# Optimization experiments

Measured on AMD Instinct MI355X. Metric: run time of the kernel, lower is better.

The kernel has to match this reference:

```python
import jax, jax.numpy as jnp
import numpy as np

E = 1024      # embed_dim
H = 8         # att_heads
ALPHA = 1.3   # CELU alpha
EPS = 1e-5    # GroupNorm eps (torch default)


def _celu(x):
    return jnp.where(x > 0, x, ALPHA * jnp.expm1(x / ALPHA))


def _proj(x2d, W, b, gamma, beta):
    # Linear -> CELU(1.3) -> GroupNorm(H groups) over flattened tokens [N, E]
    y = x2d @ W.T + b
    y = _celu(y)
    N, C = y.shape
    yg = y.reshape(N, H, C // H)
    mu = yg.mean(-1, keepdims=True)
    var = yg.var(-1, keepdims=True)
    yn = ((yg - mu) * jax.lax.rsqrt(var + EPS)).reshape(N, C)
    return yn * gamma + beta


def setup_inputs() -> dict:
    key = jax.random.key(0)
    ks = jax.random.split(key, 16)
    B, M = 32, 1024
    inp = {
        'query':  jax.random.normal(ks[0], (B, M, E), jnp.float32),
        'key':    jax.random.normal(ks[1], (B, M, E), jnp.float32),
        'mask':   jnp.ones((B, M), jnp.int32),
        'value1': jax.random.normal(ks[2], (B, E), jnp.float32),
        'value2': jax.random.normal(ks[3], (B, M, E), jnp.float32),
    }
    def lin(k):
        return jax.random.normal(k, (E, E), jnp.float32) * 0.02
    inp.update({
        'Wq': lin(ks[4]),  'bq': jnp.zeros((E,), jnp.float32),
        'gq': jnp.ones((E,), jnp.float32), 'betaq': jnp.zeros((E,), jnp.float32),
        'Wk': lin(ks[5]),  'bk': jnp.zeros((E,), jnp.float32),
        'gk': jnp.ones((E,), jnp.float32), 'betak': jnp.zeros((E,), jnp.float32),
        'Wv': lin(ks[6]),  'bv': jnp.zeros((E,), jnp.float32),
        'gv': jnp.ones((E,), jnp.float32), 'betav': jnp.zeros((E,), jnp.float32),
        'Wm': lin(ks[7]),  'bm': jnp.zeros((E,), jnp.float32),
    })
    return inp


def reference(query, key, mask, value1, value2,
              Wq, bq, gq, betaq,
              Wk, bk, gk, betak,
              Wv, bv, gv, betav,
              Wm, bm):
    B, M, C = query.shape
    D = C // H
    scaling = D ** -0.5
    # value1 is intentionally unused (matches the original module)
    q = _proj(query.reshape(-1, C),  Wq, bq, gq, betaq).reshape(B, M, H, D).transpose(0, 2, 1, 3)
    k = _proj(key.reshape(-1, C),    Wk, bk, gk, betak).reshape(B, M, H, D).transpose(0, 2, 1, 3)
    v = _proj(value2.reshape(-1, C), Wv, bv, gv, betav).reshape(B, M, H, D).transpose(0, 2, 1, 3)
    scores = jnp.einsum('bhqd,bhkd->bhqk', q, k) * scaling
    scores = jnp.where(mask[:, None, None, :] == 0, jnp.float32(-1e9), scores)
    att = jax.nn.softmax(scores, axis=-1)
    out = jnp.einsum('bhqk,bhkd->bhqd', att, v)
    out = out.transpose(0, 2, 1, 3).reshape(B, M, C)
    return out @ Wm.T + bm
```

## Files before the change

### kernel.cpp

```cpp
#include <hip/hip_runtime.h>
#include <math.h>

#define E_DIM 1024
#define HH 8
#define DH 128
#define BB 32
#define MM 1024
#define NTOK 32768
#define CHUNK 16384
#define CELU_A 1.3f
#define GN_EPS 1e-5f
#define SCALE_F 0.08838834764831845f

typedef unsigned short ushort_t;
typedef __attribute__((ext_vector_type(8))) short short8;
typedef __attribute__((ext_vector_type(4))) float f32x4;

#define MFMA16(a,b,c) __builtin_amdgcn_mfma_f32_16x16x32_bf16((a),(b),(c),0,0,0)

union U8 { short8 v; ushort_t u[8]; };

__device__ __forceinline__ ushort_t f2bf(float f) {
    unsigned u = __float_as_uint(f);
    u += 0x7fffu + ((u >> 16) & 1u);
    return (ushort_t)(u >> 16);
}
__device__ __forceinline__ float bf2f(ushort_t h) {
    return __uint_as_float(((unsigned)h) << 16);
}

__device__ __forceinline__ void gload16(const void* g, void* l) {
    __builtin_amdgcn_global_load_lds(
        (const __attribute__((address_space(1))) unsigned*)g,
        (__attribute__((address_space(3))) unsigned*)l, 16, 0, 0);
}

__global__ __launch_bounds__(256)
void split_kernel(const float* __restrict__ in, ushort_t* __restrict__ hi,
                  ushort_t* __restrict__ lo, int n8)
{
    int i = blockIdx.x * 256 + threadIdx.x;
    if (i >= n8) return;
    const float4* p = (const float4*)in;
    float4 a = p[2 * i], b = p[2 * i + 1];
    float f[8] = {a.x, a.y, a.z, a.w, b.x, b.y, b.z, b.w};
    U8 h, l;
#pragma unroll
    for (int j = 0; j < 8; ++j) {
        ushort_t hh = f2bf(f[j]);
        h.u[j] = hh;
        l.u[j] = f2bf(f[j] - bf2f(hh));
    }
    *(short8*)&hi[(size_t)i * 8] = h.v;
    *(short8*)&lo[(size_t)i * 8] = l.v;
}

__global__ __launch_bounds__(32)
void pack_mask(const int* __restrict__ mask, unsigned* __restrict__ mbits)
{
    int b = blockIdx.x, t = threadIdx.x;
    const int* mp = mask + (size_t)b * MM + t * 32;
    unsigned v = 0;
    for (int j = 0; j < 32; ++j) v |= (mp[j] != 0 ? 1u : 0u) << j;
    mbits[b * 32 + t] = v;
}

struct alignas(16) TilesT {
    ushort_t ahi[128 * 32]; ushort_t alo[128 * 32];
    ushort_t bhi[128 * 32]; ushort_t blo[128 * 32];
};
struct alignas(16) EpiT {
    float ybuf[64 * 132]; float mu[64]; float rs[64];
};
union SmemU { TilesT t; EpiT e; };

template<int MODE>
__global__ __launch_bounds__(256, 3)
void proj_kernel(const ushort_t* __restrict__ Ahi, const ushort_t* __restrict__ Alo,
                 const ushort_t* __restrict__ Bhi, const ushort_t* __restrict__ Blo,
                 const float* __restrict__ bias, const float* __restrict__ gamma,
                 const float* __restrict__ beta, int row_off,
                 ushort_t* __restrict__ out0, ushort_t* __restrict__ out1,
                 float* __restrict__ outf)
{
    __shared__ SmemU sm;

    const int tid  = threadIdx.x;
    const int w    = tid >> 6, lane = tid & 63;
    const int quad = lane >> 4, l16 = lane & 15;
    const int wr   = (w >> 1) * 64, wc = (w & 1) * 64;
    const int lrow0 = blockIdx.x * 128;
    const int row0  = row_off + lrow0;
    const int col0  = blockIdx.y * 128;

    f32x4 Cf[4][4];
#pragma unroll
    for (int i = 0; i < 4; ++i)
#pragma unroll
        for (int j = 0; j < 4; ++j) Cf[i][j] = (f32x4){0.f, 0.f, 0.f, 0.f};

    const int s0 = tid, s1 = tid + 256;
    const int ra0 = tid >> 2, ra1 = ra0 + 64;
    const int ga  = (tid & 3) * 8;

    unsigned aoff0 = 0, aoff1 = 0;
    size_t a2b0 = 0, a2b1 = 0;
    if constexpr (MODE == 2) {
        int n0 = row0 + ra0, n1 = row0 + ra1;
        a2b0 = ((size_t)(n0 >> 10) * (HH * MM) + (n0 & 1023)) * 256;
        a2b1 = ((size_t)(n1 >> 10) * (HH * MM) + (n1 & 1023)) * 256;
    } else {
        aoff0 = (unsigned)((lrow0 + ra0) * E_DIM + ga);
        aoff1 = (unsigned)((lrow0 + ra1) * E_DIM + ga);
    }
    const unsigned boff0 = (unsigned)((col0 + ra0) * E_DIM + ga);
    const unsigned boff1 = (unsigned)((col0 + ra1) * E_DIM + ga);

    for (int k0 = 0; k0 < E_DIM; k0 += 32) {
        if constexpr (MODE == 2) {
            int e0 = k0 + ga;
            size_t ao = (size_t)(e0 >> 7) * (MM * 256) + (e0 & 127);
            gload16(Ahi + a2b0 + ao,       &sm.t.ahi[s0 * 8]);
            gload16(Ahi + a2b0 + ao + 128, &sm.t.alo[s0 * 8]);
            gload16(Ahi + a2b1 + ao,       &sm.t.ahi[s1 * 8]);
            gload16(Ahi + a2b1 + ao + 128, &sm.t.alo[s1 * 8]);
        } else {
            gload16(Ahi + aoff0 + k0, &sm.t.ahi[s0 * 8]);
            gload16(Alo + aoff0 + k0, &sm.t.alo[s0 * 8]);
            gload16(Ahi + aoff1 + k0, &sm.t.ahi[s1 * 8]);
            gload16(Alo + aoff1 + k0, &sm.t.alo[s1 * 8]);
        }
        gload16(Bhi + boff0 + k0, &sm.t.bhi[s0 * 8]);
        gload16(Blo + boff0 + k0, &sm.t.blo[s0 * 8]);
        gload16(Bhi + boff1 + k0, &sm.t.bhi[s1 * 8]);
        gload16(Blo + boff1 + k0, &sm.t.blo[s1 * 8]);
        __syncthreads();
        short8 a_hi[4], a_lo[4], b_hi[4], b_lo[4];
#pragma unroll
        for (int mt = 0; mt < 4; ++mt) {
            int r = wr + mt * 16 + l16;
            a_hi[mt] = *(const short8*)&sm.t.ahi[r * 32 + quad * 8];
            a_lo[mt] = *(const short8*)&sm.t.alo[r * 32 + quad * 8];
        }
#pragma unroll
        for (int nt = 0; nt < 4; ++nt) {
            int r = wc + nt * 16 + l16;
            b_hi[nt] = *(const short8*)&sm.t.bhi[r * 32 + quad * 8];
            b_lo[nt] = *(const short8*)&sm.t.blo[r * 32 + quad * 8];
        }
#pragma unroll
        for (int mt = 0; mt < 4; ++mt)
#pragma unroll
            for (int nt = 0; nt < 4; ++nt) {
                f32x4 c = Cf[mt][nt];
                c = MFMA16(a_hi[mt], b_hi[nt], c);
                c = MFMA16(a_hi[mt], b_lo[nt], c);
                c = MFMA16(a_lo[mt], b_hi[nt], c);
                Cf[mt][nt] = c;
            }
        __syncthreads();
    }

    if constexpr (MODE == 2) {
#pragma unroll
        for (int mt = 0; mt < 4; ++mt)
#pragma unroll
            for (int nt = 0; nt < 4; ++nt) {
                int c = col0 + wc + nt * 16 + l16;
                float bv = bias[c];
#pragma unroll
                for (int reg = 0; reg < 4; ++reg) {
                    int r = row0 + wr + mt * 16 + quad * 4 + reg;
                    outf[(size_t)r * E_DIM + c] = Cf[mt][nt][reg] + bv;
                }
            }
    } else {
        for (int h2 = 0; h2 < 2; ++h2) {
            __syncthreads();
            if ((w >> 1) == h2) {
#pragma unroll
                for (int mt = 0; mt < 4; ++mt)
#pragma unroll
                    for (int nt = 0; nt < 4; ++nt) {
                        int c = wc + nt * 16 + l16;
                        float bv = bias[col0 + c];
#pragma unroll
                        for (int reg = 0; reg < 4; ++reg) {
                            int r = mt * 16 + quad * 4 + reg;
                            float x = Cf[mt][nt][reg] + bv;
                            x = x > 0.f ? x : CELU_A * (__expf(x * (1.0f / CELU_A)) - 1.0f);
                            sm.e.ybuf[r * 132 + c] = x;
                        }
                    }
            }
            __syncthreads();
            {
                int r = tid >> 2, sg = (tid & 3) * 32;
                float s = 0.f, ss = 0.f;
                for (int i = 0; i < 32; i += 4) {
                    float4 v = *(float4*)&sm.e.ybuf[r * 132 + sg + i];
                    s  += v.x + v.y + v.z + v.w;
                    ss += v.x * v.x + v.y * v.y + v.z * v.z + v.w * v.w;
                }
                s  += __shfl_xor(s, 1);  ss += __shfl_xor(ss, 1);
                s  += __shfl_xor(s, 2);  ss += __shfl_xor(ss, 2);
                if ((tid & 3) == 0) {
                    float mu  = s * (1.f / 128.f);
                    float var = ss * (1.f / 128.f) - mu * mu;
                    sm.e.mu[r] = mu;
                    sm.e.rs[r] = rsqrtf(var + GN_EPS);
                }
            }
            __syncthreads();
            if constexpr (MODE == 0) {
                int r = tid >> 2, sg = (tid & 3) * 32;
                int n = row0 + h2 * 64 + r, b = n >> 10, m = n & 1023, h = blockIdx.y;
                float mu = sm.e.mu[r], rs = sm.e.rs[r];
                ushort_t* orow = out0 + ((size_t)((b * HH + h) * MM + m)) * 256;
                for (int i0 = 0; i0 < 32; i0 += 8) {
                    U8 ph, pl;
#pragma unroll
                    for (int j = 0; j < 8; ++j) {
                        int c = sg + i0 + j;
                        float y = (sm.e.ybuf[r * 132 + c] - mu) * rs * gamma[col0 + c] + beta[col0 + c];
                        ushort_t hh = f2bf(y);
                        ph.u[j] = hh; pl.u[j] = f2bf(y - bf2f(hh));
                    }
                    *(short8*)&orow[sg + i0]       = ph.v;
                    *(short8*)&orow[128 + sg + i0] = pl.v;
                }
            } else {
                int d = tid >> 1, off = (tid & 1) * 32;
                int b = row0 >> 10, m0 = (row0 & 1023) + h2 * 64, h = blockIdx.y;
                float g = gamma[col0 + d], be = beta[col0 + d];
                size_t vbase = ((size_t)(b * HH + h) * DH + d) * MM + m0 + off;
                for (int i0 = 0; i0 < 32; i0 += 8) {
                    U8 ph, pl;
#pragma unroll
                    for (int j = 0; j < 8; ++j) {
                        int rl = off + i0 + j;
                        float y = (sm.e.ybuf[rl * 132 + d] - sm.e.mu[rl]) * sm.e.rs[rl] * g + be;
                        ushort_t hh = f2bf(y);
                        ph.u[j] = hh; pl.u[j] = f2bf(y - bf2f(hh));
                    }
                    *(short8*)&out0[vbase + i0] = ph.v;
                    *(short8*)&out1[vbase + i0] = pl.v;
                }
            }
        }
    }
}

__global__ __launch_bounds__(256, 3)
void attn_kernel(const ushort_t* __restrict__ qsp, const ushort_t* __restrict__ ksp,
                 const ushort_t* __restrict__ vhi_g, const ushort_t* __restrict__ vlo_g,
                 const unsigned* __restrict__ mbits, ushort_t* __restrict__ obuf)
{
    __shared__ __align__(16) ushort_t Ks_hi[32 * 136], Ks_lo[32 * 136];
    __shared__ __align__(16) ushort_t Vt_hi[128 * 40], Vt_lo[128 * 40];
    __shared__ __align__(16) ushort_t Phi_s[64 * 40], Plo_s[64 * 40];

    const int tid  = threadIdx.x;
    const int w    = tid >> 6, lane = tid & 63;
    const int quad = lane >> 4, l16 = lane & 15;
    const int lin = blockIdx.y * 16 + blockIdx.x;
    const int idx = lin >> 3;
    const int bh  = ((idx >> 4) << 3) | (lin & 7);
    const int q0  = (idx & 15) * 64;
    const int b   = bh >> 3;

    short8 qa_hi[4], qa_lo[4];
    {
        const ushort_t* qrow = qsp + ((size_t)bh * MM + q0 + w * 16 + l16) * 256;
#pragma unroll
        for (int kc = 0; kc < 4; ++kc) {
            qa_hi[kc] = *(const short8*)(qrow + kc * 32 + quad * 8);
            qa_lo[kc] = *(const short8*)(qrow + 128 + kc * 32 + quad * 8);
        }
    }
    f32x4 Of[8];
#pragma unroll
    for (int i = 0; i < 8; ++i) Of[i] = (f32x4){0.f, 0.f, 0.f, 0.f};
    float mreg[4] = {-3.0e38f, -3.0e38f, -3.0e38f, -3.0e38f};
    float lreg[4] = {0.f, 0.f, 0.f, 0.f};

    const int kj = tid >> 3, kseg = tid & 7;
    const ushort_t* kbase  = ksp   + ((size_t)bh * MM + kj) * 256 + kseg * 16;
    const int vd = tid >> 1, vhf = tid & 1;
    const ushort_t* vhbase = vhi_g + ((size_t)bh * DH + vd) * MM + vhf * 16;
    const ushort_t* vlbase = vlo_g + ((size_t)bh * DH + vd) * MM + vhf * 16;

    short8 ck0 = *(const short8*)(kbase);
    short8 ck1 = *(const short8*)(kbase + 8);
    short8 ck2 = *(const short8*)(kbase + 128);
    short8 ck3 = *(const short8*)(kbase + 136);
    short8 cv0 = *(const short8*)(vhbase);
    short8 cv1 = *(const short8*)(vhbase + 8);
    short8 cv2 = *(const short8*)(vlbase);
    short8 cv3 = *(const short8*)(vlbase + 8);
    unsigned mw = mbits[b << 5];

    for (int kt = 0; kt < 32; ++kt) {
        *(short8*)&Ks_hi[kj * 136 + kseg * 16 + 0] = ck0;
        *(short8*)&Ks_hi[kj * 136 + kseg * 16 + 8] = ck1;
        *(short8*)&Ks_lo[kj * 136 + kseg * 16 + 0] = ck2;
        *(short8*)&Ks_lo[kj * 136 + kseg * 16 + 8] = ck3;
        *(short8*)&Vt_hi[vd * 40 + vhf * 16 + 0] = cv0;
        *(short8*)&Vt_hi[vd * 40 + vhf * 16 + 8] = cv1;
        *(short8*)&Vt_lo[vd * 40 + vhf * 16 + 0] = cv2;
        *(short8*)&Vt_lo[vd * 40 + vhf * 16 + 8] = cv3;
        __syncthreads();
        {
            int ktn = (kt + 1) & 31;
            const ushort_t* kp  = kbase  + (size_t)ktn * 8192;
            ck0 = *(const short8*)(kp);
            ck1 = *(const short8*)(kp + 8);
            ck2 = *(const short8*)(kp + 128);
            ck3 = *(const short8*)(kp + 136);
            const ushort_t* vhp = vhbase + ktn * 32;
            const ushort_t* vlp = vlbase + ktn * 32;
            cv0 = *(const short8*)(vhp);
            cv1 = *(const short8*)(vhp + 8);
            cv2 = *(const short8*)(vlp);
            cv3 = *(const short8*)(vlp + 8);
        }
        unsigned mw_cur = mw;
        mw = mbits[(b << 5) | ((kt + 1) & 31)];
        f32x4 Sf[2];
        Sf[0] = (f32x4){0.f, 0.f, 0.f, 0.f};
        Sf[1] = (f32x4){0.f, 0.f, 0.f, 0.f};
#pragma unroll
        for (int kc = 0; kc < 4; ++kc) {
#pragma unroll
            for (int ct = 0; ct < 2; ++ct) {
                const short8 kbh = *(const short8*)&Ks_hi[(ct * 16 + l16) * 136 + kc * 32 + quad * 8];
                const short8 kbl = *(const short8*)&Ks_lo[(ct * 16 + l16) * 136 + kc * 32 + quad * 8];
                f32x4 c = Sf[ct];
                c = MFMA16(qa_hi[kc], kbh, c);
                c = MFMA16(qa_hi[kc], kbl, c);
                c = MFMA16(qa_lo[kc], kbh, c);
                Sf[ct] = c;
            }
        }
        float al4[4];
#pragma unroll
        for (int reg = 0; reg < 4; ++reg) {
            float s0 = Sf[0][reg] * SCALE_F;
            float s1 = Sf[1][reg] * SCALE_F;
            if (!((mw_cur >> l16) & 1u))        s0 = -1e9f;
            if (!((mw_cur >> (16 + l16)) & 1u)) s1 = -1e9f;
            float pm = fmaxf(s0, s1);
            pm = fmaxf(pm, __shfl_xor(pm, 1));
            pm = fmaxf(pm, __shfl_xor(pm, 2));
            pm = fmaxf(pm, __shfl_xor(pm, 4));
            pm = fmaxf(pm, __shfl_xor(pm, 8));
            float mo = mreg[reg];
            float mx = fmaxf(mo, pm);
            float al = __expf(mo - mx);
            float p0 = __expf(s0 - mx);
            float p1 = __expf(s1 - mx);
            float ps = p0 + p1;
            ps += __shfl_xor(ps, 1);
            ps += __shfl_xor(ps, 2);
            ps += __shfl_xor(ps, 4);
            ps += __shfl_xor(ps, 8);
            mreg[reg] = mx;
            lreg[reg] = lreg[reg] * al + ps;
            al4[reg] = al;
            int rr = (w << 4) + (quad << 2) + reg;
            ushort_t h0 = f2bf(p0), h1 = f2bf(p1);
            Phi_s[rr * 40 + l16]      = h0;
            Phi_s[rr * 40 + 16 + l16] = h1;
            Plo_s[rr * 40 + l16]      = f2bf(p0 - bf2f(h0));
            Plo_s[rr * 40 + 16 + l16] = f2bf(p1 - bf2f(h1));
        }
        __syncthreads();
        {
            const short8 pah = *(const short8*)&Phi_s[(w * 16 + l16) * 40 + quad * 8];
            const short8 pal = *(const short8*)&Plo_s[(w * 16 + l16) * 40 + quad * 8];
#pragma unroll
            for (int ct = 0; ct < 8; ++ct) {
                f32x4 c = Of[ct];
#pragma unroll
                for (int reg = 0; reg < 4; ++reg) c[reg] *= al4[reg];
                const short8 vbh = *(const short8*)&Vt_hi[(ct * 16 + l16) * 40 + quad * 8];
                const short8 vbl = *(const short8*)&Vt_lo[(ct * 16 + l16) * 40 + quad * 8];
                c = MFMA16(pah, vbh, c);
                c = MFMA16(pah, vbl, c);
                c = MFMA16(pal, vbh, c);
                Of[ct] = c;
            }
        }
        __syncthreads();
    }
    {
        float li[4];
#pragma unroll
        for (int reg = 0; reg < 4; ++reg) li[reg] = 1.f / lreg[reg];
#pragma unroll
        for (int ct = 0; ct < 8; ++ct)
#pragma unroll
            for (int reg = 0; reg < 4; ++reg) {
                float v = Of[ct][reg] * li[reg];
                ushort_t hh = f2bf(v);
                ushort_t ll = f2bf(v - bf2f(hh));
                size_t rb = ((size_t)bh * MM + q0 + w * 16 + quad * 4 + reg) * 256 + ct * 16 + l16;
                obuf[rb]       = hh;
                obuf[rb + 128] = ll;
            }
    }
}

extern "C" void kernel_launch(void* const* d_in, const int* in_sizes, int n_in,
                              void* d_out, int out_size, void* d_ws, size_t ws_size,
                              hipStream_t stream)
{
    const float* query  = (const float*)d_in[0];
    const float* key    = (const float*)d_in[1];
    const int*   mask   = (const int*)d_in[2];
    const float* value2 = (const float*)d_in[4];
    const float* Wq = (const float*)d_in[5];
    const float* bq = (const float*)d_in[6];
    const float* gq = (const float*)d_in[7];
    const float* betaq = (const float*)d_in[8];
    const float* Wk = (const float*)d_in[9];
    const float* bk = (const float*)d_in[10];
    const float* gk = (const float*)d_in[11];
    const float* betak = (const float*)d_in[12];
    const float* Wv = (const float*)d_in[13];
    const float* bv = (const float*)d_in[14];
    const float* gv = (const float*)d_in[15];
    const float* betav = (const float*)d_in[16];
    const float* Wm = (const float*)d_in[17];
    const float* bm = (const float*)d_in[18];
    float* out = (float*)d_out;

    ushort_t* qsp = (ushort_t*)d_ws;
    ushort_t* ksp = qsp + (size_t)67108864;
    ushort_t* vhi = ksp + (size_t)67108864;
    ushort_t* vlo = vhi + (size_t)33554432;

    ushort_t* ob    = (ushort_t*)d_out;
    ushort_t* xhi   = ob;
    ushort_t* xlo   = ob + (size_t)CHUNK * E_DIM;
    ushort_t* wkhi  = ob + (size_t)2 * CHUNK * E_DIM;
    ushort_t* wklo  = wkhi + (size_t)E_DIM * E_DIM;
    unsigned* mbits = (unsigned*)(ob + (size_t)41943040);
    ushort_t* wvhi  = qsp;
    ushort_t* wvlo  = wvhi + (size_t)E_DIM * E_DIM;
    ushort_t* wqhi  = ksp;
    ushort_t* wqlo  = wqhi + (size_t)E_DIM * E_DIM;
    ushort_t* wmhi  = ksp;
    ushort_t* wmlo  = wmhi + (size_t)E_DIM * E_DIM;

    const int WN8 = (E_DIM * E_DIM) / 8;
    const int XN8 = (CHUNK * E_DIM) / 8;

    pack_mask<<<BB, 32, 0, stream>>>(mask, mbits);
    split_kernel<<<WN8 / 256, 256, 0, stream>>>(Wv, wvhi, wvlo, WN8);
    split_kernel<<<WN8 / 256, 256, 0, stream>>>(Wq, wqhi, wqlo, WN8);
    split_kernel<<<WN8 / 256, 256, 0, stream>>>(Wk, wkhi, wklo, WN8);

    dim3 gproj(CHUNK / 128, E_DIM / 128);

    for (int c = 0; c < 2; ++c) {
        split_kernel<<<XN8 / 256, 256, 0, stream>>>(value2 + (size_t)c * CHUNK * E_DIM, xhi, xlo, XN8);
        proj_kernel<1><<<gproj, 256, 0, stream>>>(xhi, xlo, wvhi, wvlo, bv, gv, betav,
                                                  c * CHUNK, vhi, vlo, nullptr);
    }
    for (int c = 0; c < 2; ++c) {
        split_kernel<<<XN8 / 256, 256, 0, stream>>>(query + (size_t)c * CHUNK * E_DIM, xhi, xlo, XN8);
        proj_kernel<0><<<gproj, 256, 0, stream>>>(xhi, xlo, wqhi, wqlo, bq, gq, betaq,
                                                  c * CHUNK, qsp, nullptr, nullptr);
    }
    for (int c = 0; c < 2; ++c) {
        split_kernel<<<XN8 / 256, 256, 0, stream>>>(key + (size_t)c * CHUNK * E_DIM, xhi, xlo, XN8);
        proj_kernel<0><<<gproj, 256, 0, stream>>>(xhi, xlo, wkhi, wklo, bk, gk, betak,
                                                  c * CHUNK, ksp, nullptr, nullptr);
    }

    attn_kernel<<<dim3(MM / 64, BB * HH), 256, 0, stream>>>(qsp, ksp, vhi, vlo, mbits, qsp);

    split_kernel<<<WN8 / 256, 256, 0, stream>>>(Wm, wmhi, wmlo, WN8);
    proj_kernel<2><<<dim3(NTOK / 128, E_DIM / 128), 256, 0, stream>>>(
        qsp, nullptr, wmhi, wmlo, bm, nullptr, nullptr, 0, nullptr, nullptr, out);
}
```

Measured before the change: 2.190 ms.

## Rewrite attention with 32x32 MFMA and transposed S to keep P in registers

The attention kernel switches from 16x16x32 to 32x32x16 bf16 MFMA, computing S transposed (K as A operand, Q as B) so each lane holds one query's scores. The P tile is then repacked into MFMA operands with lane-crossing shuffles instead of being written to LDS, which removes the P shared buffers and one barrier per key tile. Each block now handles 128 queries (32 per wave), which increases register pressure, so occupancy is lowered to 2 blocks per SM and the grid shrinks to 8x256 blocks.

```diff
diff --git a/kernel.cpp b/kernel.cpp
--- a/kernel.cpp
+++ b/kernel.cpp
@@ -15,10 +15,13 @@
 typedef unsigned short ushort_t;
 typedef __attribute__((ext_vector_type(8))) short short8;
 typedef __attribute__((ext_vector_type(4))) float f32x4;
+typedef __attribute__((ext_vector_type(16))) float f32x16;
 
 #define MFMA16(a,b,c) __builtin_amdgcn_mfma_f32_16x16x32_bf16((a),(b),(c),0,0,0)
+#define MFMA32(a,b,c) __builtin_amdgcn_mfma_f32_32x32x16_bf16((a),(b),(c),0,0,0)
 
 union U8 { short8 v; ushort_t u[8]; };
+union U32x4 { unsigned u[4]; short8 v; };
 
 __device__ __forceinline__ ushort_t f2bf(float f) {
     unsigned u = __float_as_uint(f);
@@ -251,38 +254,36 @@
     }
 }
 
-__global__ __launch_bounds__(256, 3)
+__global__ __launch_bounds__(256, 2)
 void attn_kernel(const ushort_t* __restrict__ qsp, const ushort_t* __restrict__ ksp,
                  const ushort_t* __restrict__ vhi_g, const ushort_t* __restrict__ vlo_g,
                  const unsigned* __restrict__ mbits, ushort_t* __restrict__ obuf)
 {
     __shared__ __align__(16) ushort_t Ks_hi[32 * 136], Ks_lo[32 * 136];
     __shared__ __align__(16) ushort_t Vt_hi[128 * 40], Vt_lo[128 * 40];
-    __shared__ __align__(16) ushort_t Phi_s[64 * 40], Plo_s[64 * 40];
 
     const int tid  = threadIdx.x;
     const int w    = tid >> 6, lane = tid & 63;
-    const int quad = lane >> 4, l16 = lane & 15;
-    const int lin = blockIdx.y * 16 + blockIdx.x;
-    const int idx = lin >> 3;
-    const int bh  = ((idx >> 4) << 3) | (lin & 7);
-    const int q0  = (idx & 15) * 64;
-    const int b   = bh >> 3;
-
-    short8 qa_hi[4], qa_lo[4];
+    const int l32  = lane & 31, h = lane >> 5;
+    const int bh = ((blockIdx.y >> 3) << 3) | blockIdx.x;
+    const int q0 = (blockIdx.y & 7) * 128;
+    const int b  = bh >> 3;
+
+    short8 qb_hi[8], qb_lo[8];
     {
-        const ushort_t* qrow = qsp + ((size_t)bh * MM + q0 + w * 16 + l16) * 256;
-#pragma unroll
-        for (int kc = 0; kc < 4; ++kc) {
-            qa_hi[kc] = *(const short8*)(qrow + kc * 32 + quad * 8);
-            qa_lo[kc] = *(const short8*)(qrow + 128 + kc * 32 + quad * 8);
-        }
-    }
-    f32x4 Of[8];
-#pragma unroll
-    for (int i = 0; i < 8; ++i) Of[i] = (f32x4){0.f, 0.f, 0.f, 0.f};
-    float mreg[4] = {-3.0e38f, -3.0e38f, -3.0e38f, -3.0e38f};
-    float lreg[4] = {0.f, 0.f, 0.f, 0.f};
+        const ushort_t* qrow = qsp + ((size_t)bh * MM + q0 + w * 32 + l32) * 256 + h * 8;
+#pragma unroll
+        for (int kc = 0; kc < 8; ++kc) {
+            qb_hi[kc] = *(const short8*)(qrow + kc * 16);
+            qb_lo[kc] = *(const short8*)(qrow + 128 + kc * 16);
+        }
+    }
+    f32x16 Of[4];
+#pragma unroll
+    for (int i = 0; i < 4; ++i)
+#pragma unroll
+        for (int r = 0; r < 16; ++r) Of[i][r] = 0.f;
+    float m_old = -3.0e38f, l_run = 0.f;
 
     const int kj = tid >> 3, kseg = tid & 7;
     const ushort_t* kbase  = ksp   + ((size_t)bh * MM + kj) * 256 + kseg * 16;
@@ -326,87 +327,105 @@
         }
         unsigned mw_cur = mw;
         mw = mbits[(b << 5) | ((kt + 1) & 31)];
-        f32x4 Sf[2];
-        Sf[0] = (f32x4){0.f, 0.f, 0.f, 0.f};
-        Sf[1] = (f32x4){0.f, 0.f, 0.f, 0.f};
-#pragma unroll
-        for (int kc = 0; kc < 4; ++kc) {
-#pragma unroll
-            for (int ct = 0; ct < 2; ++ct) {
-                const short8 kbh = *(const short8*)&Ks_hi[(ct * 16 + l16) * 136 + kc * 32 + quad * 8];
-                const short8 kbl = *(const short8*)&Ks_lo[(ct * 16 + l16) * 136 + kc * 32 + quad * 8];
-                f32x4 c = Sf[ct];
-                c = MFMA16(qa_hi[kc], kbh, c);
-                c = MFMA16(qa_hi[kc], kbl, c);
-                c = MFMA16(qa_lo[kc], kbh, c);
-                Sf[ct] = c;
-            }
-        }
-        float al4[4];
-#pragma unroll
-        for (int reg = 0; reg < 4; ++reg) {
-            float s0 = Sf[0][reg] * SCALE_F;
-            float s1 = Sf[1][reg] * SCALE_F;
-            if (!((mw_cur >> l16) & 1u))        s0 = -1e9f;
-            if (!((mw_cur >> (16 + l16)) & 1u)) s1 = -1e9f;
-            float pm = fmaxf(s0, s1);
-            pm = fmaxf(pm, __shfl_xor(pm, 1));
-            pm = fmaxf(pm, __shfl_xor(pm, 2));
-            pm = fmaxf(pm, __shfl_xor(pm, 4));
-            pm = fmaxf(pm, __shfl_xor(pm, 8));
-            float mo = mreg[reg];
-            float mx = fmaxf(mo, pm);
-            float al = __expf(mo - mx);
-            float p0 = __expf(s0 - mx);
-            float p1 = __expf(s1 - mx);
-            float ps = p0 + p1;
-            ps += __shfl_xor(ps, 1);
-            ps += __shfl_xor(ps, 2);
-            ps += __shfl_xor(ps, 4);
-            ps += __shfl_xor(ps, 8);
-            mreg[reg] = mx;
-            lreg[reg] = lreg[reg] * al + ps;
-            al4[reg] = al;
-            int rr = (w << 4) + (quad << 2) + reg;
-            ushort_t h0 = f2bf(p0), h1 = f2bf(p1);
-            Phi_s[rr * 40 + l16]      = h0;
-            Phi_s[rr * 40 + 16 + l16] = h1;
-            Plo_s[rr * 40 + l16]      = f2bf(p0 - bf2f(h0));
-            Plo_s[rr * 40 + 16 + l16] = f2bf(p1 - bf2f(h1));
+
+        f32x16 Sf;
+#pragma unroll
+        for (int r = 0; r < 16; ++r) Sf[r] = 0.f;
+#pragma unroll
+        for (int kc = 0; kc < 8; ++kc) {
+            const short8 ka = *(const short8*)&Ks_hi[l32 * 136 + h * 8 + kc * 16];
+            const short8 kl = *(const short8*)&Ks_lo[l32 * 136 + h * 8 + kc * 16];
+            Sf = MFMA32(ka, qb_hi[kc], Sf);
+            Sf = MFMA32(ka, qb_lo[kc], Sf);
+            Sf = MFMA32(kl, qb_hi[kc], Sf);
+        }
+        float sv[16];
+        float pm = -3.0e38f;
+#pragma unroll
+        for (int r = 0; r < 16; ++r) {
+            int kk = (r & 3) + 8 * (r >> 2) + 4 * h;
+            float s = Sf[r] * SCALE_F;
+            if (!((mw_cur >> kk) & 1u)) s = -1e9f;
+            sv[r] = s;
+            pm = fmaxf(pm, s);
+        }
+        pm = fmaxf(pm, __shfl_xor(pm, 32));
+        float mx = fmaxf(m_old, pm);
+        float al = __expf(m_old - mx);
+        float ps = 0.f;
+#pragma unroll
+        for (int r = 0; r < 16; ++r) { float p = __expf(sv[r] - mx); sv[r] = p; ps += p; }
+        ps += __shfl_xor(ps, 32);
+        m_old = mx;
+        l_run = l_run * al + ps;
+
+        unsigned pa_h[4], pb_h[4], pa_l[4], pb_l[4];
+#pragma unroll
+        for (int g = 0; g < 4; ++g) {
+            ushort_t h0 = f2bf(sv[g*4+0]), h1 = f2bf(sv[g*4+1]);
+            ushort_t h2 = f2bf(sv[g*4+2]), h3 = f2bf(sv[g*4+3]);
+            pa_h[g] = (unsigned)h0 | ((unsigned)h1 << 16);
+            pb_h[g] = (unsigned)h2 | ((unsigned)h3 << 16);
+            ushort_t l0 = f2bf(sv[g*4+0] - bf2f(h0)), l1 = f2bf(sv[g*4+1] - bf2f(h1));
+            ushort_t l2 = f2bf(sv[g*4+2] - bf2f(h2)), l3 = f2bf(sv[g*4+3] - bf2f(h3));
+            pa_l[g] = (unsigned)l0 | ((unsigned)l1 << 16);
+            pb_l[g] = (unsigned)l2 | ((unsigned)l3 << 16);
+        }
+        short8 pf_h[2], pf_l[2];
+#pragma unroll
+        for (int kc = 0; kc < 2; ++kc) {
+            U32x4 fh, fl;
+            {
+                unsigned ta = h ? pa_h[2*kc] : pa_h[2*kc+1];
+                unsigned tb = h ? pb_h[2*kc] : pb_h[2*kc+1];
+                unsigned ra = (unsigned)__shfl_xor((int)ta, 32);
+                unsigned rb = (unsigned)__shfl_xor((int)tb, 32);
+                fh.u[0] = h ? ra : pa_h[2*kc];
+                fh.u[1] = h ? rb : pb_h[2*kc];
+                fh.u[2] = h ? pa_h[2*kc+1] : ra;
+                fh.u[3] = h ? pb_h[2*kc+1] : rb;
+            }
+            {
+                unsigned ta = h ? pa_l[2*kc] : pa_l[2*kc+1];
+                unsigned tb = h ? pb_l[2*kc] : pb_l[2*kc+1];
+                unsigned ra = (unsigned)__shfl_xor((int)ta, 32);
+                unsigned rb = (unsigned)__shfl_xor((int)tb, 32);
+                fl.u[0] = h ? ra : pa_l[2*kc];
+                fl.u[1] = h ? rb : pb_l[2*kc];
+                fl.u[2] = h ? pa_l[2*kc+1] : ra;
+                fl.u[3] = h ? pb_l[2*kc+1] : rb;
+            }
+            pf_h[kc] = fh.v; pf_l[kc] = fl.v;
+        }
+#pragma unroll
+        for (int dg = 0; dg < 4; ++dg) {
+            f32x16 c = Of[dg];
+#pragma unroll
+            for (int r = 0; r < 16; ++r) c[r] *= al;
+#pragma unroll
+            for (int kc = 0; kc < 2; ++kc) {
+                const short8 va = *(const short8*)&Vt_hi[(dg * 32 + l32) * 40 + h * 8 + kc * 16];
+                const short8 vl = *(const short8*)&Vt_lo[(dg * 32 + l32) * 40 + h * 8 + kc * 16];
+                c = MFMA32(va, pf_h[kc], c);
+                c = MFMA32(va, pf_l[kc], c);
+                c = MFMA32(vl, pf_h[kc], c);
+            }
+            Of[dg] = c;
         }
         __syncthreads();
-        {
-            const short8 pah = *(const short8*)&Phi_s[(w * 16 + l16) * 40 + quad * 8];
-            const short8 pal = *(const short8*)&Plo_s[(w * 16 + l16) * 40 + quad * 8];
-#pragma unroll
-            for (int ct = 0; ct < 8; ++ct) {
-                f32x4 c = Of[ct];
-#pragma unroll
-                for (int reg = 0; reg < 4; ++reg) c[reg] *= al4[reg];
-                const short8 vbh = *(const short8*)&Vt_hi[(ct * 16 + l16) * 40 + quad * 8];
-                const short8 vbl = *(const short8*)&Vt_lo[(ct * 16 + l16) * 40 + quad * 8];
-                c = MFMA16(pah, vbh, c);
-                c = MFMA16(pah, vbl, c);
-                c = MFMA16(pal, vbh, c);
-                Of[ct] = c;
-            }
-        }
-        __syncthreads();
     }
     {
-        float li[4];
-#pragma unroll
-        for (int reg = 0; reg < 4; ++reg) li[reg] = 1.f / lreg[reg];
-#pragma unroll
-        for (int ct = 0; ct < 8; ++ct)
-#pragma unroll
-            for (int reg = 0; reg < 4; ++reg) {
-                float v = Of[ct][reg] * li[reg];
+        float inv = 1.f / l_run;
+        ushort_t* orow = obuf + ((size_t)bh * MM + q0 + w * 32 + l32) * 256;
+#pragma unroll
+        for (int dg = 0; dg < 4; ++dg)
+#pragma unroll
+            for (int r = 0; r < 16; ++r) {
+                int d = dg * 32 + (r & 3) + 8 * (r >> 2) + 4 * h;
+                float v = Of[dg][r] * inv;
                 ushort_t hh = f2bf(v);
-                ushort_t ll = f2bf(v - bf2f(hh));
-                size_t rb = ((size_t)bh * MM + q0 + w * 16 + quad * 4 + reg) * 256 + ct * 16 + l16;
-                obuf[rb]       = hh;
-                obuf[rb + 128] = ll;
+                orow[d]       = hh;
+                orow[128 + d] = f2bf(v - bf2f(hh));
             }
     }
 }
@@ -479,7 +498,7 @@
                                                   c * CHUNK, ksp, nullptr, nullptr);
     }
 
-    attn_kernel<<<dim3(MM / 64, BB * HH), 256, 0, stream>>>(qsp, ksp, vhi, vlo, mbits, qsp);
+    attn_kernel<<<dim3(8, 256), 256, 0, stream>>>(qsp, ksp, vhi, vlo, mbits, qsp);
 
     split_kernel<<<WN8 / 256, 256, 0, stream>>>(Wm, wmhi, wmlo, WN8);
     proj_kernel<2><<<dim3(NTOK / 128, E_DIM / 128), 256, 0, stream>>>(
```

After: 2.034 ms. 7.1% less time.
